# Performance work log

Hardware: AMD Instinct MI355X
Metric: run time of the kernel (lower is better)

Reference implementation:

```python
import jax, jax.numpy as jnp
import numpy as np

DIM = 64      # d_model, expand=1 -> d_inner = DIM
H_IN = 128
W_IN = 128
DS = 8        # d_state
DTR = 4       # dt_rank = ceil(DIM/16)
DCONV = 4     # conv kernel size
NDIR = 4      # bimamba v6: h-fwd, h-bwd, w-fwd, w-bwd


def layernorm(x, g, b, eps=1e-5):
    m = x.mean(-1, keepdims=True)
    v = x.var(-1, keepdims=True)
    return (x - m) / jnp.sqrt(v + eps) * g + b


def causal_conv(x, w, b):
    # x: (B, L, D), w: (D, 1, K) depthwise, causal left pad
    xt = x.transpose(0, 2, 1)  # (B, D, L)
    y = jax.lax.conv_general_dilated(xt, w, (1,), [(DCONV - 1, 0)],
                                     feature_group_count=xt.shape[1])
    return y.transpose(0, 2, 1) + b


def selective_scan(u, delta, A, Bm, Cm, D):
    # u,delta: (B,L,D); A: (D,N); Bm,Cm: (B,L,N); D: (D,)
    dA = jnp.exp(delta[..., None] * A)                       # (B,L,D,N)
    dBu = delta[..., None] * Bm[:, :, None, :] * u[..., None]

    def comb(c1, c2):
        a1, b1 = c1
        a2, b2 = c2
        return a1 * a2, a2 * b1 + b2

    _, hs = jax.lax.associative_scan(comb, (dA, dBu), axis=1)  # (B,L,D,N)
    return jnp.einsum('bldn,bln->bld', hs, Cm) + u * D


def setup_inputs() -> dict:
    key = jax.random.key(0)
    ks = jax.random.split(key, 12)
    s = 0.02
    inp = {
        'input': jax.random.normal(ks[0], (2, DIM, H_IN, W_IN), jnp.float32),
        'ln_g': jnp.ones((DIM,), jnp.float32),
        'ln_b': jnp.zeros((DIM,), jnp.float32),
        'in_proj_w': jax.random.normal(ks[1], (2 * DIM, DIM), jnp.float32) * s,
        'conv_w': jax.random.normal(ks[2], (NDIR, DIM, 1, DCONV), jnp.float32) * s,
        'conv_b': jnp.zeros((NDIR, DIM), jnp.float32),
        'xproj_w': jax.random.normal(ks[3], (NDIR, DTR + 2 * DS, DIM), jnp.float32) * s,
        'dtproj_w': jax.random.normal(ks[4], (NDIR, DIM, DTR), jnp.float32) * s,
        'dtproj_b': jax.random.normal(ks[5], (NDIR, DIM), jnp.float32) * 0.1,
        'A_log': jnp.broadcast_to(jnp.log(jnp.arange(1.0, DS + 1.0, dtype=jnp.float32)),
                                  (NDIR, DIM, DS)).copy(),
        'D_skip': jnp.ones((NDIR, DIM), jnp.float32),
        'on_g': jnp.ones((DIM,), jnp.float32),
        'on_b': jnp.zeros((DIM,), jnp.float32),
        'out_proj_w': jax.random.normal(ks[6], (DIM, DIM), jnp.float32) * s,
    }
    return inp


def reference(input, ln_g, ln_b, in_proj_w, conv_w, conv_b, xproj_w,
              dtproj_w, dtproj_b, A_log, D_skip, on_g, on_b, out_proj_w):
    B, C, H, W = input.shape
    L = H * W
    seq = input.reshape(B, C, L).transpose(0, 2, 1)           # b (h w) c
    seq = layernorm(seq, ln_g, ln_b)
    xz = seq @ in_proj_w.T                                    # (B,L,2D)
    x, z = jnp.split(xz, 2, axis=-1)

    ar = jnp.arange(L)
    perm = (ar % H) * W + ar // H    # (h w) -> (w h)
    inv = (ar % W) * H + ar // W     # (w h) -> (h w)

    dirs = [(None, False), (None, True), (perm, False), (perm, True)]
    y_sum = jnp.zeros_like(x)
    for i, (p, rev) in enumerate(dirs):
        xd = x if p is None else x[:, p]
        if rev:
            xd = jnp.flip(xd, 1)
        xd = jax.nn.silu(causal_conv(xd, conv_w[i], conv_b[i]))
        dbl = xd @ xproj_w[i].T
        dt, Bm, Cm = jnp.split(dbl, [DTR, DTR + DS], axis=-1)
        dt = jax.nn.softplus(dt @ dtproj_w[i].T + dtproj_b[i])
        A = -jnp.exp(A_log[i])
        yd = selective_scan(xd, dt, A, Bm, Cm, D_skip[i])
        if rev:
            yd = jnp.flip(yd, 1)
        if p is not None:
            yd = yd[:, inv]
        y_sum = y_sum + yd

    y = y_sum / float(NDIR)                 # if_devide_out=True
    y = layernorm(y, on_g, on_b)            # use_norm=True
    y = y * jax.nn.silu(z)                  # gate
    out = y @ out_proj_w.T
    return out.transpose(0, 2, 1).reshape(B, C, H, W) + input
```

## Files before the change

kernel.cpp:

```cpp
#include <hip/hip_runtime.h>
#include <hip/hip_bf16.h>
#include <hip/hip_fp16.h>
#include <cstdint>
#include <cstddef>

#define L_TOT 16384
#define B_SZ 2
#define NROW (B_SZ * L_TOT)
#define CHUNK 32
#define NCH (L_TOT / CHUNK)

static constexpr size_t SLOT_XD  = (size_t)NROW * 64;
static constexpr size_t SLOT_DBC = (size_t)NROW * 20;
static constexpr size_t SLOT_SDT = (size_t)B_SZ * 64 * NCH;
static constexpr size_t SLOT_HC  = (size_t)B_SZ * NCH * 64 * 8;

union H8pack { float4 f4; __half2 h2[4]; };
union H4pack { float2 f2; __half2 h2[2]; };

typedef _Float16 h2v __attribute__((ext_vector_type(2)));
#if __has_builtin(__builtin_amdgcn_fdot2)
#define FDOT2(a, b, c) __builtin_amdgcn_fdot2((a), (b), (c), false)
#else
#define FDOT2(a, b, c) fmaf((float)(a)[0], (float)(b)[0], fmaf((float)(a)[1], (float)(b)[1], (c)))
#endif

__device__ __forceinline__ int tau_map(int dir, int s) {
  int j = (dir & 1) ? (L_TOT - 1 - s) : s;
  if (dir >= 2) j = ((j & 127) << 7) | (j >> 7);
  return j;
}
__device__ __forceinline__ float silu_f(float x) { return x / (1.f + __expf(-x)); }
__device__ __forceinline__ float softplus_f(float x) {
  return fmaxf(x, 0.f) + __logf(1.f + __expf(-fabsf(x)));
}

__global__ void __launch_bounds__(256)
k_ln_inproj(const float* __restrict__ inp, const float* __restrict__ lng,
            const float* __restrict__ lnb, const float* __restrict__ W,
            float* __restrict__ xout, float* __restrict__ zout) {
  __shared__ float xt[64 * 65];
  __shared__ float wrk[8448];
  const int t = threadIdx.x;
  const int lane = t & 63;
  const int w = t >> 6;
  const int b = blockIdx.x >> 8;
  const int l0 = (blockIdx.x & 255) << 6;
  const float* ip = inp + (size_t)b * 64 * L_TOT + l0 + lane;
#pragma unroll 4
  for (int cc = 0; cc < 16; ++cc) {
    int c = cc * 4 + w;
    xt[lane * 65 + c] = ip[(size_t)c * L_TOT];
  }
  __syncthreads();
  {
    float s1 = 0.f, s2 = 0.f;
    const int c0 = w * 16;
#pragma unroll
    for (int cc = 0; cc < 16; ++cc) {
      float v = xt[lane * 65 + c0 + cc];
      s1 += v; s2 = fmaf(v, v, s2);
    }
    wrk[w * 64 + lane] = s1;
    wrk[256 + w * 64 + lane] = s2;
  }
  __syncthreads();
  if (t < 64) {
    float s1 = wrk[t] + wrk[64 + t] + wrk[128 + t] + wrk[192 + t];
    float s2 = wrk[256 + t] + wrk[320 + t] + wrk[384 + t] + wrk[448 + t];
    float m = s1 * 0.015625f;
    float var = s2 * 0.015625f - m * m;
    wrk[512 + t] = m;
    wrk[576 + t] = rsqrtf(var + 1e-5f);
  }
  __syncthreads();
  {
    const float mv = wrk[512 + lane], rv = wrk[576 + lane];
#pragma unroll 4
    for (int k = 0; k < 16; ++k) {
      int c = w + 4 * k;
      float g = lng[c], bb = lnb[c];
      float v = xt[lane * 65 + c];
      xt[lane * 65 + c] = (v - mv) * rv * g + bb;
    }
  }
  __syncthreads();
#pragma unroll 4
  for (int rep = 0; rep < 32; ++rep) {
    int j = rep * 4 + w;
    wrk[j * 65 + lane] = W[(size_t)j * 64 + lane];
  }
  __syncthreads();
  const int rg = lane & 15;
  const int jg = lane >> 4;
  const int j0 = w * 32 + jg * 8;
  const int r0 = rg * 4;
  float acc[4][8] = {};
#pragma unroll 2
  for (int c = 0; c < 64; ++c) {
    float xv[4], wv[8];
#pragma unroll
    for (int i = 0; i < 4; ++i) xv[i] = xt[(r0 + i) * 65 + c];
#pragma unroll
    for (int jj = 0; jj < 8; ++jj) wv[jj] = wrk[(j0 + jj) * 65 + c];
#pragma unroll
    for (int i = 0; i < 4; ++i)
#pragma unroll
      for (int jj = 0; jj < 8; ++jj) acc[i][jj] = fmaf(xv[i], wv[jj], acc[i][jj]);
  }
  __syncthreads();
#pragma unroll
  for (int i = 0; i < 4; ++i)
#pragma unroll
    for (int jj = 0; jj < 8; ++jj) wrk[(r0 + i) * 132 + j0 + jj] = acc[i][jj];
  __syncthreads();
  float* xo = xout + ((size_t)b * L_TOT + l0) * 64;
  float* zo = zout + ((size_t)b * L_TOT + l0) * 64;
#pragma unroll 4
  for (int rep = 0; rep < 16; ++rep) {
    int r = rep * 4 + w;
    xo[(size_t)r * 64 + lane] = wrk[r * 132 + lane];
    zo[(size_t)r * 64 + lane] = wrk[r * 132 + 64 + lane];
  }
}

__global__ void __launch_bounds__(256)
k_convscan(const float* __restrict__ xbuf, const float* __restrict__ cw,
           const float* __restrict__ cb, const float* __restrict__ xpw,
           const float* __restrict__ dtw, const float* __restrict__ dtbias,
           const float* __restrict__ alog,
           float* __restrict__ xd_base, float* __restrict__ dbc_base,
           __half* __restrict__ hcb, __half* __restrict__ sdtb, int dir_base) {
  __shared__ __align__(16) _Float16 xh[67 * 70];
  __shared__ __align__(16) _Float16 wt[20 * 70];
  __shared__ __align__(16) float dbl[64 * 20];
  const int t = threadIdx.x;
  const int lane = t & 63;
  const int w = t >> 6;
  const int slot = blockIdx.y;
  const int dir = dir_base + slot;
  const int blk = blockIdx.x;
  const int b = blk >> 8;
  const int s0 = (blk & 255) << 6;
  const float* xb = xbuf + (size_t)b * L_TOT * 64;
#pragma unroll 1
  for (int i = w; i < 67; i += 4) {
    int s = s0 - 3 + i;
    float v = 0.f;
    if (s >= 0) v = xb[(size_t)tau_map(dir, s) * 64 + lane];
    xh[i * 70 + lane] = (_Float16)v;
  }
#pragma unroll
  for (int jj = 0; jj < 5; ++jj) {
    int j = jj * 4 + w;
    wt[j * 70 + lane] = (_Float16)xpw[((size_t)dir * 20 + j) * 64 + lane];
  }
  __syncthreads();
  float wk[4];
#pragma unroll
  for (int k = 0; k < 4; ++k) wk[k] = cw[(dir * 64 + lane) * 4 + k];
  const float bconv = cb[dir * 64 + lane];
  float u[16];
  float* xdp = xd_base + (size_t)slot * SLOT_XD + ((size_t)b * L_TOT + s0) * 64;
#pragma unroll 4
  for (int rr = 0; rr < 16; ++rr) {
    const int r = rr * 4 + w;
    float acc = bconv;
#pragma unroll
    for (int k = 0; k < 4; ++k) acc = fmaf(wk[k], (float)xh[(r + k) * 70 + lane], acc);
    acc = silu_f(acc);
    u[rr] = acc;
    xdp[(size_t)r * 64 + lane] = acc;
  }
  __syncthreads();
#pragma unroll 4
  for (int rr = 0; rr < 16; ++rr) xh[(rr * 4 + w) * 70 + lane] = (_Float16)u[rr];
  __syncthreads();
  {
    float acc5[5] = {0.f, 0.f, 0.f, 0.f, 0.f};
    const _Float16* xr = xh + lane * 70;
#pragma unroll 4
    for (int c2 = 0; c2 < 32; ++c2) {
      h2v xv = *(const h2v*)(xr + 2 * c2);
#pragma unroll
      for (int jj = 0; jj < 5; ++jj) {
        h2v wv = *(const h2v*)(wt + (w * 5 + jj) * 70 + 2 * c2);
        acc5[jj] = FDOT2(xv, wv, acc5[jj]);
      }
    }
#pragma unroll
    for (int jj = 0; jj < 5; ++jj) dbl[lane * 20 + w * 5 + jj] = acc5[jj];
  }
  __syncthreads();
  float* dbp = dbc_base + (size_t)slot * SLOT_DBC + ((size_t)b * L_TOT + s0) * 20;
#pragma unroll
  for (int i = t; i < 1280; i += 256) dbp[i] = dbl[i];
  {
    const int w2 = w & 1;
    const int ng = (w >> 1) << 2;
    const int d = lane;
    const int ch = (s0 >> 5) + w2;
    const float* asrc = alog + ((size_t)dir * 64 + d) * 8;
    float a4[4];
#pragma unroll
    for (int k = 0; k < 4; ++k) a4[k] = -__expf(asrc[ng + k]);
    const float a0 = (ng == 0) ? a4[0] : -__expf(asrc[0]);
    bool pw = true;
#pragma unroll
    for (int k = 0; k < 4; ++k) {
      float tgt = (float)(ng + k + 1) * a0;
      pw = pw && (fabsf(a4[k] - tgt) <= 1e-3f * fabsf(tgt));
    }
    float wdt[4];
#pragma unroll
    for (int r = 0; r < 4; ++r) wdt[r] = dtw[((size_t)dir * 64 + d) * 4 + r];
    const float bia = dtbias[dir * 64 + d];
    const _Float16* xs = xh + (w2 * 32) * 70;
    const float* ds = dbl + (w2 * 32) * 20;
    float h[4] = {0.f, 0.f, 0.f, 0.f};
    float sdt = 0.f;
    if (pw) {
#pragma unroll 8
      for (int s = 0; s < CHUNK; ++s) {
        float uu = (float)xs[s * 70 + d];
        float4 dd = *(const float4*)(ds + s * 20);
        float4 bb = *(const float4*)(ds + s * 20 + 4 + ng);
        float dt = bia;
        dt = fmaf(dd.x, wdt[0], dt); dt = fmaf(dd.y, wdt[1], dt);
        dt = fmaf(dd.z, wdt[2], dt); dt = fmaf(dd.w, wdt[3], dt);
        dt = softplus_f(dt);
        sdt += dt;
        float du = dt * uu;
        float p = __expf(dt * a0);
        float p2 = p * p, p4 = p2 * p2;
        float e0, e1, e2, e3;
        if (ng == 0) { e0 = p; e1 = p2; e2 = p2 * p; e3 = p4; }
        else { e0 = p4 * p; e1 = p4 * p2; e2 = e1 * p; e3 = p4 * p4; }
        h[0] = fmaf(e0, h[0], du * bb.x);
        h[1] = fmaf(e1, h[1], du * bb.y);
        h[2] = fmaf(e2, h[2], du * bb.z);
        h[3] = fmaf(e3, h[3], du * bb.w);
      }
    } else {
#pragma unroll 8
      for (int s = 0; s < CHUNK; ++s) {
        float uu = (float)xs[s * 70 + d];
        float4 dd = *(const float4*)(ds + s * 20);
        float4 bb = *(const float4*)(ds + s * 20 + 4 + ng);
        float dt = bia;
        dt = fmaf(dd.x, wdt[0], dt); dt = fmaf(dd.y, wdt[1], dt);
        dt = fmaf(dd.z, wdt[2], dt); dt = fmaf(dd.w, wdt[3], dt);
        dt = softplus_f(dt);
        sdt += dt;
        float du = dt * uu;
        h[0] = fmaf(__expf(dt * a4[0]), h[0], du * bb.x);
        h[1] = fmaf(__expf(dt * a4[1]), h[1], du * bb.y);
        h[2] = fmaf(__expf(dt * a4[2]), h[2], du * bb.z);
        h[3] = fmaf(__expf(dt * a4[3]), h[3], du * bb.w);
      }
    }
    if (ng == 0)
      sdtb[(size_t)slot * SLOT_SDT + ((size_t)b * 64 + d) * NCH + ch] = __float2half(sdt);
    H4pack pk;
    pk.h2[0] = __floats2half2_rn(h[0], h[1]);
    pk.h2[1] = __floats2half2_rn(h[2], h[3]);
    *(float2*)(hcb + (size_t)slot * SLOT_HC +
               (((size_t)b * NCH + ch) * 64 + d) * 8 + ng) = pk.f2;
  }
}

__global__ void __launch_bounds__(512)
k_scan2(__half* __restrict__ hcb, const __half* __restrict__ sdtb,
        const float* __restrict__ alog, int dir_base) {
  const int t = threadIdx.x;
  const int d = blockIdx.x >> 3;
  const int n = blockIdx.x & 7;
  const int slot = blockIdx.y;
  const int dir = dir_base + slot;
  const int b = blockIdx.z;
  const float a = -__expf(alog[((size_t)dir * 64 + d) * 8 + n]);
  __half* hcp = hcb + (size_t)slot * SLOT_HC + (size_t)b * NCH * 512;
  const __half* sdp = sdtb + (size_t)slot * SLOT_SDT + ((size_t)b * 64 + d) * NCH;
  float e = __expf(a * __half2float(sdp[t]));
  float v = __half2float(hcp[((size_t)t * 64 + d) * 8 + n]);
  __shared__ float sE[NCH], sV[NCH];
  sE[t] = e; sV[t] = v;
  __syncthreads();
#pragma unroll
  for (int off = 1; off < NCH; off <<= 1) {
    float pe = 1.f, pv = 0.f;
    if (t >= off) { pe = sE[t - off]; pv = sV[t - off]; }
    __syncthreads();
    v = fmaf(e, pv, v);
    e = e * pe;
    sE[t] = e; sV[t] = v;
    __syncthreads();
  }
  const float hs = (t == 0) ? 0.f : sV[t - 1];
  hcp[((size_t)t * 64 + d) * 8 + n] = __float2half(hs);
}

__global__ void __launch_bounds__(256, 4)
k_scan3(const float* xd_in, const float* __restrict__ dbc_base,
        const __half* __restrict__ hcb, const float* __restrict__ alog,
        const float* __restrict__ dtw, const float* __restrict__ dtbias,
        const float* __restrict__ dsk, float* y_base,
        int dir_base, int scatter) {
  __shared__ __align__(16) float rpl[4 * CHUNK * 20];
  const int t = threadIdx.x;
  const int w = t >> 6;
  const int d = t & 63;
  const int ch = blockIdx.x * 4 + w;
  const int slot = blockIdx.y;
  const int dir = dir_base + slot;
  const int b = blockIdx.z;
  const float* rblk = dbc_base + (size_t)slot * SLOT_DBC +
                      ((size_t)b * L_TOT + (size_t)blockIdx.x * 4 * CHUNK) * 20;
#pragma unroll 1
  for (int i = t; i < 4 * CHUNK * 20; i += 256) rpl[i] = rblk[i];
  __syncthreads();
  const float* rp = rpl + w * CHUNK * 20;
  float a[8];
#pragma unroll
  for (int n = 0; n < 8; ++n) a[n] = -__expf(alog[((size_t)dir * 64 + d) * 8 + n]);
  const float a0 = a[0];
  bool pw = true;
#pragma unroll
  for (int n = 0; n < 8; ++n) {
    float tgt = (float)(n + 1) * a0;
    pw = pw && (fabsf(a[n] - tgt) <= 1e-3f * fabsf(tgt));
  }
  float wdt[4];
#pragma unroll
  for (int r = 0; r < 4; ++r) wdt[r] = dtw[((size_t)dir * 64 + d) * 4 + r];
  const float bia = dtbias[dir * 64 + d];
  const float Dv = dsk[dir * 64 + d];
  const float* up = xd_in + (size_t)slot * SLOT_XD + ((size_t)b * L_TOT + ch * CHUNK) * 64;
  float h[8];
  {
    H8pack pk;
    pk.f4 = *(const float4*)(hcb + (size_t)slot * SLOT_HC +
                             (((size_t)b * NCH + ch) * 64 + d) * 8);
#pragma unroll
    for (int k = 0; k < 4; ++k) {
      h[2 * k] = __low2float(pk.h2[k]);
      h[2 * k + 1] = __high2float(pk.h2[k]);
    }
  }
  const int sbase = ch * CHUNK;
  if (pw) {
#pragma unroll 8
    for (int s = 0; s < CHUNK; ++s) {
      float u = up[s * 64 + d];
      float4 dd = *(const float4*)(rp + s * 20);
      float4 b0 = *(const float4*)(rp + s * 20 + 4);
      float4 b1 = *(const float4*)(rp + s * 20 + 8);
      float4 c0 = *(const float4*)(rp + s * 20 + 12);
      float4 c1 = *(const float4*)(rp + s * 20 + 16);
      float dt = bia;
      dt = fmaf(dd.x, wdt[0], dt); dt = fmaf(dd.y, wdt[1], dt);
      dt = fmaf(dd.z, wdt[2], dt); dt = fmaf(dd.w, wdt[3], dt);
      dt = softplus_f(dt);
      float du = dt * u;
      float p = __expf(dt * a0);
      float p2 = p * p, p3 = p2 * p, p4 = p2 * p2;
      float p5 = p4 * p, p6 = p4 * p2, p7 = p4 * p3, p8 = p4 * p4;
      h[0] = fmaf(p,  h[0], du * b0.x);
      h[1] = fmaf(p2, h[1], du * b0.y);
      h[2] = fmaf(p3, h[2], du * b0.z);
      h[3] = fmaf(p4, h[3], du * b0.w);
      h[4] = fmaf(p5, h[4], du * b1.x);
      h[5] = fmaf(p6, h[5], du * b1.y);
      h[6] = fmaf(p7, h[6], du * b1.z);
      h[7] = fmaf(p8, h[7], du * b1.w);
      float y = u * Dv;
      y = fmaf(c0.x, h[0], y); y = fmaf(c0.y, h[1], y);
      y = fmaf(c0.z, h[2], y); y = fmaf(c0.w, h[3], y);
      y = fmaf(c1.x, h[4], y); y = fmaf(c1.y, h[5], y);
      y = fmaf(c1.z, h[6], y); y = fmaf(c1.w, h[7], y);
      if (scatter) {
        int l = tau_map(dir, sbase + s);
        y_base[((size_t)b * L_TOT + l) * 64 + d] += y;
      } else {
        y_base[(size_t)slot * SLOT_XD + ((size_t)b * L_TOT + sbase + s) * 64 + d] = y;
      }
    }
  } else {
#pragma unroll 8
    for (int s = 0; s < CHUNK; ++s) {
      float u = up[s * 64 + d];
      float4 dd = *(const float4*)(rp + s * 20);
      float4 b0 = *(const float4*)(rp + s * 20 + 4);
      float4 b1 = *(const float4*)(rp + s * 20 + 8);
      float4 c0 = *(const float4*)(rp + s * 20 + 12);
      float4 c1 = *(const float4*)(rp + s * 20 + 16);
      float dt = bia;
      dt = fmaf(dd.x, wdt[0], dt); dt = fmaf(dd.y, wdt[1], dt);
      dt = fmaf(dd.z, wdt[2], dt); dt = fmaf(dd.w, wdt[3], dt);
      dt = softplus_f(dt);
      float du = dt * u;
      float y = u * Dv;
      float bv[8] = {b0.x, b0.y, b0.z, b0.w, b1.x, b1.y, b1.z, b1.w};
      float cv[8] = {c0.x, c0.y, c0.z, c0.w, c1.x, c1.y, c1.z, c1.w};
#pragma unroll
      for (int n = 0; n < 8; ++n) {
        h[n] = fmaf(__expf(dt * a[n]), h[n], du * bv[n]);
        y = fmaf(cv[n], h[n], y);
      }
      if (scatter) {
        int l = tau_map(dir, sbase + s);
        y_base[((size_t)b * L_TOT + l) * 64 + d] += y;
      } else {
        y_base[(size_t)slot * SLOT_XD + ((size_t)b * L_TOT + sbase + s) * 64 + d] = y;
      }
    }
  }
}

__global__ void __launch_bounds__(256)
k_final(const float* __restrict__ ybase, const float* __restrict__ zbuf,
        const float* __restrict__ ong, const float* __restrict__ onb,
        const float* __restrict__ OW, const float* __restrict__ inp,
        float* __restrict__ out, int gather) {
  __shared__ float xt[64 * 65];
  __shared__ float tzw[64 * 65];
  __shared__ float st[640];
  const int t = threadIdx.x;
  const int lane = t & 63;
  const int w = t >> 6;
  const int b = blockIdx.x >> 8;
  const int l0 = (blockIdx.x & 255) << 6;
#pragma unroll 2
  for (int rep = 0; rep < 16; ++rep) {
    int r = rep * 4 + w;
    int l = l0 + r;
    float acc;
    if (gather) {
      acc = 0.f;
#pragma unroll
      for (int dir = 0; dir < 4; ++dir) {
        int s = tau_map(dir, l);
        acc += ybase[(size_t)dir * SLOT_XD + ((size_t)b * L_TOT + s) * 64 + lane];
      }
    } else {
      acc = ybase[((size_t)b * L_TOT + l) * 64 + lane];
    }
    xt[r * 65 + lane] = acc * 0.25f;
    tzw[r * 65 + lane] = zbuf[((size_t)b * L_TOT + l) * 64 + lane];
  }
  __syncthreads();
  {
    float s1 = 0.f, s2 = 0.f;
    const int c0 = w * 16;
#pragma unroll
    for (int cc = 0; cc < 16; ++cc) {
      float v = xt[lane * 65 + c0 + cc];
      s1 += v; s2 = fmaf(v, v, s2);
    }
    st[w * 64 + lane] = s1;
    st[256 + w * 64 + lane] = s2;
  }
  __syncthreads();
  if (t < 64) {
    float s1 = st[t] + st[64 + t] + st[128 + t] + st[192 + t];
    float s2 = st[256 + t] + st[320 + t] + st[384 + t] + st[448 + t];
    float m = s1 * 0.015625f;
    float var = s2 * 0.015625f - m * m;
    st[512 + t] = m;
    st[576 + t] = rsqrtf(var + 1e-5f);
  }
  __syncthreads();
  {
    const float mv = st[512 + lane], rv = st[576 + lane];
#pragma unroll 4
    for (int k = 0; k < 16; ++k) {
      int c = w + 4 * k;
      float g = ong[c], bb = onb[c];
      float v = xt[lane * 65 + c];
      float zz = tzw[lane * 65 + c];
      xt[lane * 65 + c] = ((v - mv) * rv * g + bb) * silu_f(zz);
    }
  }
  __syncthreads();
#pragma unroll 4
  for (int rep = 0; rep < 16; ++rep) {
    int j = rep * 4 + w;
    tzw[j * 65 + lane] = OW[(size_t)j * 64 + lane];
  }
  __syncthreads();
  const int rg = lane & 15;
  const int jg = lane >> 4;
  const int j0 = w * 16 + jg * 4;
  const int r0 = rg * 4;
  float acc[4][4] = {};
#pragma unroll 2
  for (int c = 0; c < 64; ++c) {
    float xv[4], wv[4];
#pragma unroll
    for (int i = 0; i < 4; ++i) xv[i] = xt[(r0 + i) * 65 + c];
#pragma unroll
    for (int jj = 0; jj < 4; ++jj) wv[jj] = tzw[(j0 + jj) * 65 + c];
#pragma unroll
    for (int i = 0; i < 4; ++i)
#pragma unroll
      for (int jj = 0; jj < 4; ++jj) acc[i][jj] = fmaf(xv[i], wv[jj], acc[i][jj]);
  }
  __syncthreads();
#pragma unroll
  for (int i = 0; i < 4; ++i)
#pragma unroll
    for (int jj = 0; jj < 4; ++jj) xt[(j0 + jj) * 65 + r0 + i] = acc[i][jj];
  __syncthreads();
#pragma unroll 4
  for (int rep = 0; rep < 16; ++rep) {
    int j = rep * 4 + w;
    size_t o = ((size_t)b * 64 + j) * L_TOT + l0 + lane;
    out[o] = xt[j * 65 + lane] + inp[o];
  }
}

extern "C" void kernel_launch(void* const* d_in, const int* in_sizes, int n_in,
                              void* d_out, int out_size, void* d_ws, size_t ws_size,
                              hipStream_t stream) {
  const float* inp    = (const float*)d_in[0];
  const float* lng    = (const float*)d_in[1];
  const float* lnb    = (const float*)d_in[2];
  const float* ipw    = (const float*)d_in[3];
  const float* cw     = (const float*)d_in[4];
  const float* cb     = (const float*)d_in[5];
  const float* xpw    = (const float*)d_in[6];
  const float* dtw    = (const float*)d_in[7];
  const float* dtbias = (const float*)d_in[8];
  const float* alog   = (const float*)d_in[9];
  const float* dsk    = (const float*)d_in[10];
  const float* ong    = (const float*)d_in[11];
  const float* onb    = (const float*)d_in[12];
  const float* opw    = (const float*)d_in[13];
  float* out = (float*)d_out;
  float* ws = (float*)d_ws;

  const size_t need_batched = (6 * SLOT_XD + 4 * SLOT_DBC) * sizeof(float) +
                              (4 * SLOT_SDT + 4 * SLOT_HC) * sizeof(__half);

  if (ws_size >= need_batched) {
    size_t off = 0;
    float* xbuf = ws + off; off += SLOT_XD;
    float* zbuf = ws + off; off += SLOT_XD;
    float* xd   = ws + off; off += 4 * SLOT_XD;
    float* dbc  = ws + off; off += 4 * SLOT_DBC;
    __half* sdt = (__half*)(ws + off); off += (4 * SLOT_SDT) / 2;
    __half* hc  = (__half*)(ws + off); off += (4 * SLOT_HC) / 2;

    k_ln_inproj<<<dim3(512), 256, 0, stream>>>(inp, lng, lnb, ipw, xbuf, zbuf);
    k_convscan<<<dim3(512, 4), 256, 0, stream>>>(xbuf, cw, cb, xpw, dtw, dtbias, alog,
                                                 xd, dbc, hc, sdt, 0);
    k_scan2<<<dim3(512, 4, B_SZ), NCH, 0, stream>>>(hc, sdt, alog, 0);
    k_scan3<<<dim3(NCH / 4, 4, B_SZ), 256, 0, stream>>>(xd, dbc, hc, alog, dtw, dtbias, dsk,
                                                        xd, 0, 0);
    k_final<<<dim3(512), 256, 0, stream>>>(xd, zbuf, ong, onb, opw, inp, out, 1);
  } else {
    size_t off = 0;
    float* xbuf = ws + off; off += SLOT_XD;
    float* zbuf = ws + off; off += SLOT_XD;
    float* ysum = ws + off; off += SLOT_XD;
    float* xd   = ws + off; off += SLOT_XD;
    float* dbc  = ws + off; off += SLOT_DBC;
    __half* sdt = (__half*)(ws + off); off += SLOT_SDT / 2 + 1;
    __half* hc  = (__half*)(ws + off); off += SLOT_HC / 2;

    hipMemsetAsync(ysum, 0, SLOT_XD * sizeof(float), stream);
    k_ln_inproj<<<dim3(512), 256, 0, stream>>>(inp, lng, lnb, ipw, xbuf, zbuf);
    for (int d2 = 0; d2 < 4; ++d2) {
      k_convscan<<<dim3(512, 1), 256, 0, stream>>>(xbuf, cw, cb, xpw, dtw, dtbias, alog,
                                                   xd, dbc, hc, sdt, d2);
      k_scan2<<<dim3(512, 1, B_SZ), NCH, 0, stream>>>(hc, sdt, alog, d2);
      k_scan3<<<dim3(NCH / 4, 1, B_SZ), 256, 0, stream>>>(xd, dbc, hc, alog, dtw, dtbias, dsk,
                                                          ysum, d2, 1);
    }
    k_final<<<dim3(512), 256, 0, stream>>>(ysum, zbuf, ong, onb, opw, inp, out, 0);
  }
}
```

Measured before the change: 129.4 us.

## Store scan intermediates in fp16 and precompute softplus dt once per element

Intermediate buffers (conv output u, B/C projections, per-direction y outputs) are now stored as fp16 instead of fp32, which roughly halves the global traffic between the conv/scan/final kernels. The dt projection and softplus are computed once in the conv kernel and written to a new fp16 buffer, so the two scan passes no longer recompute them. This adds a 64-wide dt write and read per row in exchange for dropping the ALU work, and it lowers precision of intermediates and of the summed outputs.

```diff
diff --git a/kernel.cpp b/kernel.cpp
--- a/kernel.cpp
+++ b/kernel.cpp
@@ -11,7 +11,9 @@
 #define NCH (L_TOT / CHUNK)
 
 static constexpr size_t SLOT_XD  = (size_t)NROW * 64;
-static constexpr size_t SLOT_DBC = (size_t)NROW * 20;
+static constexpr size_t HSLOT_XD = (size_t)NROW * 64;
+static constexpr size_t HSLOT_BC = (size_t)NROW * 16;
+static constexpr size_t HSLOT_DT = (size_t)NROW * 64;
 static constexpr size_t SLOT_SDT = (size_t)B_SZ * 64 * NCH;
 static constexpr size_t SLOT_HC  = (size_t)B_SZ * NCH * 64 * 8;
 
@@ -129,7 +131,8 @@
            const float* __restrict__ cb, const float* __restrict__ xpw,
            const float* __restrict__ dtw, const float* __restrict__ dtbias,
            const float* __restrict__ alog,
-           float* __restrict__ xd_base, float* __restrict__ dbc_base,
+           __half* __restrict__ xd_base, __half* __restrict__ bc_base,
+           __half* __restrict__ dtb_base,
            __half* __restrict__ hcb, __half* __restrict__ sdtb, int dir_base) {
   __shared__ __align__(16) _Float16 xh[67 * 70];
   __shared__ __align__(16) _Float16 wt[20 * 70];
@@ -161,7 +164,7 @@
   for (int k = 0; k < 4; ++k) wk[k] = cw[(dir * 64 + lane) * 4 + k];
   const float bconv = cb[dir * 64 + lane];
   float u[16];
-  float* xdp = xd_base + (size_t)slot * SLOT_XD + ((size_t)b * L_TOT + s0) * 64;
+  __half* xdp = xd_base + (size_t)slot * HSLOT_XD + ((size_t)b * L_TOT + s0) * 64;
 #pragma unroll 4
   for (int rr = 0; rr < 16; ++rr) {
     const int r = rr * 4 + w;
@@ -170,7 +173,7 @@
     for (int k = 0; k < 4; ++k) acc = fmaf(wk[k], (float)xh[(r + k) * 70 + lane], acc);
     acc = silu_f(acc);
     u[rr] = acc;
-    xdp[(size_t)r * 64 + lane] = acc;
+    xdp[(size_t)r * 64 + lane] = __float2half(acc);
   }
   __syncthreads();
 #pragma unroll 4
@@ -192,9 +195,31 @@
     for (int jj = 0; jj < 5; ++jj) dbl[lane * 20 + w * 5 + jj] = acc5[jj];
   }
   __syncthreads();
-  float* dbp = dbc_base + (size_t)slot * SLOT_DBC + ((size_t)b * L_TOT + s0) * 20;
-#pragma unroll
-  for (int i = t; i < 1280; i += 256) dbp[i] = dbl[i];
+  {
+    __half* bcp = bc_base + (size_t)slot * HSLOT_BC + ((size_t)b * L_TOT + s0) * 16;
+#pragma unroll
+    for (int i = t; i < 1024; i += 256) {
+      int r = i >> 4, j = i & 15;
+      bcp[i] = __float2half(dbl[r * 20 + 4 + j]);
+    }
+  }
+  __half* dtp = dtb_base + (size_t)slot * HSLOT_DT + ((size_t)b * L_TOT + s0) * 64;
+  {
+    float wdt[4];
+#pragma unroll
+    for (int r = 0; r < 4; ++r) wdt[r] = dtw[((size_t)dir * 64 + lane) * 4 + r];
+    const float bia = dtbias[dir * 64 + lane];
+#pragma unroll 4
+    for (int rr = 0; rr < 16; ++rr) {
+      const int r = rr * 4 + w;
+      float dt = bia;
+#pragma unroll
+      for (int q = 0; q < 4; ++q) dt = fmaf(dbl[r * 20 + q], wdt[q], dt);
+      dt = softplus_f(dt);
+      dtp[(size_t)r * 64 + lane] = __float2half(dt);
+    }
+  }
+  __syncthreads();
   {
     const int w2 = w & 1;
     const int ng = (w >> 1) << 2;
@@ -211,24 +236,17 @@
       float tgt = (float)(ng + k + 1) * a0;
       pw = pw && (fabsf(a4[k] - tgt) <= 1e-3f * fabsf(tgt));
     }
-    float wdt[4];
-#pragma unroll
-    for (int r = 0; r < 4; ++r) wdt[r] = dtw[((size_t)dir * 64 + d) * 4 + r];
-    const float bia = dtbias[dir * 64 + d];
     const _Float16* xs = xh + (w2 * 32) * 70;
     const float* ds = dbl + (w2 * 32) * 20;
+    const __half* dts = dtp + (size_t)(w2 * 32) * 64;
     float h[4] = {0.f, 0.f, 0.f, 0.f};
     float sdt = 0.f;
     if (pw) {
 #pragma unroll 8
       for (int s = 0; s < CHUNK; ++s) {
         float uu = (float)xs[s * 70 + d];
-        float4 dd = *(const float4*)(ds + s * 20);
+        float dt = __half2float(dts[s * 64 + d]);
         float4 bb = *(const float4*)(ds + s * 20 + 4 + ng);
-        float dt = bia;
-        dt = fmaf(dd.x, wdt[0], dt); dt = fmaf(dd.y, wdt[1], dt);
-        dt = fmaf(dd.z, wdt[2], dt); dt = fmaf(dd.w, wdt[3], dt);
-        dt = softplus_f(dt);
         sdt += dt;
         float du = dt * uu;
         float p = __expf(dt * a0);
@@ -245,12 +263,8 @@
 #pragma unroll 8
       for (int s = 0; s < CHUNK; ++s) {
         float uu = (float)xs[s * 70 + d];
-        float4 dd = *(const float4*)(ds + s * 20);
+        float dt = __half2float(dts[s * 64 + d]);
         float4 bb = *(const float4*)(ds + s * 20 + 4 + ng);
-        float dt = bia;
-        dt = fmaf(dd.x, wdt[0], dt); dt = fmaf(dd.y, wdt[1], dt);
-        dt = fmaf(dd.z, wdt[2], dt); dt = fmaf(dd.w, wdt[3], dt);
-        dt = softplus_f(dt);
         sdt += dt;
         float du = dt * uu;
         h[0] = fmaf(__expf(dt * a4[0]), h[0], du * bb.x);
@@ -301,12 +315,12 @@
 }
 
 __global__ void __launch_bounds__(256, 4)
-k_scan3(const float* xd_in, const float* __restrict__ dbc_base,
-        const __half* __restrict__ hcb, const float* __restrict__ alog,
-        const float* __restrict__ dtw, const float* __restrict__ dtbias,
-        const float* __restrict__ dsk, float* y_base,
+k_scan3(const __half* __restrict__ xd_in, const __half* __restrict__ bc_base,
+        const __half* __restrict__ dtb_base, const __half* __restrict__ hcb,
+        const float* __restrict__ alog, const float* __restrict__ dsk,
+        float* __restrict__ ysum_f, __half* __restrict__ y_h,
         int dir_base, int scatter) {
-  __shared__ __align__(16) float rpl[4 * CHUNK * 20];
+  __shared__ __align__(16) float rpl[4 * CHUNK * 16];
   const int t = threadIdx.x;
   const int w = t >> 6;
   const int d = t & 63;
@@ -314,12 +328,12 @@
   const int slot = blockIdx.y;
   const int dir = dir_base + slot;
   const int b = blockIdx.z;
-  const float* rblk = dbc_base + (size_t)slot * SLOT_DBC +
-                      ((size_t)b * L_TOT + (size_t)blockIdx.x * 4 * CHUNK) * 20;
-#pragma unroll 1
-  for (int i = t; i < 4 * CHUNK * 20; i += 256) rpl[i] = rblk[i];
-  __syncthreads();
-  const float* rp = rpl + w * CHUNK * 20;
+  const __half* bcblk = bc_base + (size_t)slot * HSLOT_BC +
+                        ((size_t)b * L_TOT + (size_t)blockIdx.x * 4 * CHUNK) * 16;
+#pragma unroll
+  for (int i = t; i < 4 * CHUNK * 16; i += 256) rpl[i] = __half2float(bcblk[i]);
+  __syncthreads();
+  const float* rp = rpl + w * CHUNK * 16;
   float a[8];
 #pragma unroll
   for (int n = 0; n < 8; ++n) a[n] = -__expf(alog[((size_t)dir * 64 + d) * 8 + n]);
@@ -330,12 +344,9 @@
     float tgt = (float)(n + 1) * a0;
     pw = pw && (fabsf(a[n] - tgt) <= 1e-3f * fabsf(tgt));
   }
-  float wdt[4];
-#pragma unroll
-  for (int r = 0; r < 4; ++r) wdt[r] = dtw[((size_t)dir * 64 + d) * 4 + r];
-  const float bia = dtbias[dir * 64 + d];
   const float Dv = dsk[dir * 64 + d];
-  const float* up = xd_in + (size_t)slot * SLOT_XD + ((size_t)b * L_TOT + ch * CHUNK) * 64;
+  const __half* up  = xd_in + (size_t)slot * HSLOT_XD + ((size_t)b * L_TOT + ch * CHUNK) * 64;
+  const __half* dtp = dtb_base + (size_t)slot * HSLOT_DT + ((size_t)b * L_TOT + ch * CHUNK) * 64;
   float h[8];
   {
     H8pack pk;
@@ -351,16 +362,12 @@
   if (pw) {
 #pragma unroll 8
     for (int s = 0; s < CHUNK; ++s) {
-      float u = up[s * 64 + d];
-      float4 dd = *(const float4*)(rp + s * 20);
-      float4 b0 = *(const float4*)(rp + s * 20 + 4);
-      float4 b1 = *(const float4*)(rp + s * 20 + 8);
-      float4 c0 = *(const float4*)(rp + s * 20 + 12);
-      float4 c1 = *(const float4*)(rp + s * 20 + 16);
-      float dt = bia;
-      dt = fmaf(dd.x, wdt[0], dt); dt = fmaf(dd.y, wdt[1], dt);
-      dt = fmaf(dd.z, wdt[2], dt); dt = fmaf(dd.w, wdt[3], dt);
-      dt = softplus_f(dt);
+      float u = __half2float(up[s * 64 + d]);
+      float dt = __half2float(dtp[s * 64 + d]);
+      float4 b0 = *(const float4*)(rp + s * 16);
+      float4 b1 = *(const float4*)(rp + s * 16 + 4);
+      float4 c0 = *(const float4*)(rp + s * 16 + 8);
+      float4 c1 = *(const float4*)(rp + s * 16 + 12);
       float du = dt * u;
       float p = __expf(dt * a0);
       float p2 = p * p, p3 = p2 * p, p4 = p2 * p2;
@@ -380,24 +387,20 @@
       y = fmaf(c1.z, h[6], y); y = fmaf(c1.w, h[7], y);
       if (scatter) {
         int l = tau_map(dir, sbase + s);
-        y_base[((size_t)b * L_TOT + l) * 64 + d] += y;
+        ysum_f[((size_t)b * L_TOT + l) * 64 + d] += y;
       } else {
-        y_base[(size_t)slot * SLOT_XD + ((size_t)b * L_TOT + sbase + s) * 64 + d] = y;
+        y_h[(size_t)slot * HSLOT_XD + ((size_t)b * L_TOT + sbase + s) * 64 + d] = __float2half(y);
       }
     }
   } else {
 #pragma unroll 8
     for (int s = 0; s < CHUNK; ++s) {
-      float u = up[s * 64 + d];
-      float4 dd = *(const float4*)(rp + s * 20);
-      float4 b0 = *(const float4*)(rp + s * 20 + 4);
-      float4 b1 = *(const float4*)(rp + s * 20 + 8);
-      float4 c0 = *(const float4*)(rp + s * 20 + 12);
-      float4 c1 = *(const float4*)(rp + s * 20 + 16);
-      float dt = bia;
-      dt = fmaf(dd.x, wdt[0], dt); dt = fmaf(dd.y, wdt[1], dt);
-      dt = fmaf(dd.z, wdt[2], dt); dt = fmaf(dd.w, wdt[3], dt);
-      dt = softplus_f(dt);
+      float u = __half2float(up[s * 64 + d]);
+      float dt = __half2float(dtp[s * 64 + d]);
+      float4 b0 = *(const float4*)(rp + s * 16);
+      float4 b1 = *(const float4*)(rp + s * 16 + 4);
+      float4 c0 = *(const float4*)(rp + s * 16 + 8);
+      float4 c1 = *(const float4*)(rp + s * 16 + 12);
       float du = dt * u;
       float y = u * Dv;
       float bv[8] = {b0.x, b0.y, b0.z, b0.w, b1.x, b1.y, b1.z, b1.w};
@@ -409,16 +412,17 @@
       }
       if (scatter) {
         int l = tau_map(dir, sbase + s);
-        y_base[((size_t)b * L_TOT + l) * 64 + d] += y;
+        ysum_f[((size_t)b * L_TOT + l) * 64 + d] += y;
       } else {
-        y_base[(size_t)slot * SLOT_XD + ((size_t)b * L_TOT + sbase + s) * 64 + d] = y;
+        y_h[(size_t)slot * HSLOT_XD + ((size_t)b * L_TOT + sbase + s) * 64 + d] = __float2half(y);
       }
     }
   }
 }
 
 __global__ void __launch_bounds__(256)
-k_final(const float* __restrict__ ybase, const float* __restrict__ zbuf,
+k_final(const __half* __restrict__ yh, const float* __restrict__ ysum,
+        const float* __restrict__ zbuf,
         const float* __restrict__ ong, const float* __restrict__ onb,
         const float* __restrict__ OW, const float* __restrict__ inp,
         float* __restrict__ out, int gather) {
@@ -440,10 +444,10 @@
 #pragma unroll
       for (int dir = 0; dir < 4; ++dir) {
         int s = tau_map(dir, l);
-        acc += ybase[(size_t)dir * SLOT_XD + ((size_t)b * L_TOT + s) * 64 + lane];
+        acc += __half2float(yh[(size_t)dir * HSLOT_XD + ((size_t)b * L_TOT + s) * 64 + lane]);
       }
     } else {
-      acc = ybase[((size_t)b * L_TOT + l) * 64 + lane];
+      acc = ysum[((size_t)b * L_TOT + l) * 64 + lane];
     }
     xt[r * 65 + lane] = acc * 0.25f;
     tzw[r * 65 + lane] = zbuf[((size_t)b * L_TOT + l) * 64 + lane];
@@ -539,44 +543,50 @@
   float* out = (float*)d_out;
   float* ws = (float*)d_ws;
 
-  const size_t need_batched = (6 * SLOT_XD + 4 * SLOT_DBC) * sizeof(float) +
-                              (4 * SLOT_SDT + 4 * SLOT_HC) * sizeof(__half);
+  const size_t half_elems = 4 * (HSLOT_XD + HSLOT_BC + HSLOT_DT + SLOT_SDT + SLOT_HC);
+  const size_t need_batched = 2 * SLOT_XD * sizeof(float) + half_elems * sizeof(__half);
 
   if (ws_size >= need_batched) {
     size_t off = 0;
     float* xbuf = ws + off; off += SLOT_XD;
     float* zbuf = ws + off; off += SLOT_XD;
-    float* xd   = ws + off; off += 4 * SLOT_XD;
-    float* dbc  = ws + off; off += 4 * SLOT_DBC;
-    __half* sdt = (__half*)(ws + off); off += (4 * SLOT_SDT) / 2;
-    __half* hc  = (__half*)(ws + off); off += (4 * SLOT_HC) / 2;
+    __half* hb = (__half*)(ws + off);
+    size_t ho = 0;
+    __half* xd  = hb + ho; ho += 4 * HSLOT_XD;
+    __half* bc  = hb + ho; ho += 4 * HSLOT_BC;
+    __half* dtb = hb + ho; ho += 4 * HSLOT_DT;
+    __half* sdt = hb + ho; ho += 4 * SLOT_SDT;
+    __half* hc  = hb + ho; ho += 4 * SLOT_HC;
 
     k_ln_inproj<<<dim3(512), 256, 0, stream>>>(inp, lng, lnb, ipw, xbuf, zbuf);
     k_convscan<<<dim3(512, 4), 256, 0, stream>>>(xbuf, cw, cb, xpw, dtw, dtbias, alog,
-                                                 xd, dbc, hc, sdt, 0);
+                                                 xd, bc, dtb, hc, sdt, 0);
     k_scan2<<<dim3(512, 4, B_SZ), NCH, 0, stream>>>(hc, sdt, alog, 0);
-    k_scan3<<<dim3(NCH / 4, 4, B_SZ), 256, 0, stream>>>(xd, dbc, hc, alog, dtw, dtbias, dsk,
-                                                        xd, 0, 0);
-    k_final<<<dim3(512), 256, 0, stream>>>(xd, zbuf, ong, onb, opw, inp, out, 1);
+    k_scan3<<<dim3(NCH / 4, 4, B_SZ), 256, 0, stream>>>(xd, bc, dtb, hc, alog, dsk,
+                                                        nullptr, xd, 0, 0);
+    k_final<<<dim3(512), 256, 0, stream>>>(xd, nullptr, zbuf, ong, onb, opw, inp, out, 1);
   } else {
     size_t off = 0;
     float* xbuf = ws + off; off += SLOT_XD;
     float* zbuf = ws + off; off += SLOT_XD;
     float* ysum = ws + off; off += SLOT_XD;
-    float* xd   = ws + off; off += SLOT_XD;
-    float* dbc  = ws + off; off += SLOT_DBC;
-    __half* sdt = (__half*)(ws + off); off += SLOT_SDT / 2 + 1;
-    __half* hc  = (__half*)(ws + off); off += SLOT_HC / 2;
+    __half* hb = (__half*)(ws + off);
+    size_t ho = 0;
+    __half* xd  = hb + ho; ho += HSLOT_XD;
+    __half* bc  = hb + ho; ho += HSLOT_BC;
+    __half* dtb = hb + ho; ho += HSLOT_DT;
+    __half* sdt = hb + ho; ho += SLOT_SDT;
+    __half* hc  = hb + ho; ho += SLOT_HC;
 
     hipMemsetAsync(ysum, 0, SLOT_XD * sizeof(float), stream);
     k_ln_inproj<<<dim3(512), 256, 0, stream>>>(inp, lng, lnb, ipw, xbuf, zbuf);
     for (int d2 = 0; d2 < 4; ++d2) {
       k_convscan<<<dim3(512, 1), 256, 0, stream>>>(xbuf, cw, cb, xpw, dtw, dtbias, alog,
-                                                   xd, dbc, hc, sdt, d2);
+                                                   xd, bc, dtb, hc, sdt, d2);
       k_scan2<<<dim3(512, 1, B_SZ), NCH, 0, stream>>>(hc, sdt, alog, d2);
-      k_scan3<<<dim3(NCH / 4, 1, B_SZ), 256, 0, stream>>>(xd, dbc, hc, alog, dtw, dtbias, dsk,
-                                                          ysum, d2, 1);
-    }
-    k_final<<<dim3(512), 256, 0, stream>>>(ysum, zbuf, ong, onb, opw, inp, out, 0);
-  }
-}
+      k_scan3<<<dim3(NCH / 4, 1, B_SZ), 256, 0, stream>>>(xd, bc, dtb, hc, alog, dsk,
+                                                          ysum, nullptr, d2, 1);
+    }
+    k_final<<<dim3(512), 256, 0, stream>>>(nullptr, ysum, zbuf, ong, onb, opw, inp, out, 0);
+  }
+}
```

Measured after the change: 125.0 us. -3.4%, faster.
